# Kernel optimization log

Hardware: AMD Instinct MI355X
Metric: run time of the kernel (lower is better)

Reference implementation:

```python
import jax, jax.numpy as jnp
import numpy as np

N = 50000
E = 500000
IN_DIM = 384
HID = 128
HEADS = 4
OUT_DIM = 384
NEG_SLOPE = 0.2


def gat_conv(x, edge_index, W, att_src, att_dst, bias):
    """PyG GATConv (concat=True, add_self_loops=True, eval mode).
    x: [N, F_in]; edge_index: [2, E] (row 0 = source j, row 1 = target i);
    W: [F_in, H*C]; att_src/att_dst: [H, C]; bias: [H*C].
    """
    n = x.shape[0]
    # add self loops
    loops = jnp.arange(n, dtype=edge_index.dtype)
    src = jnp.concatenate([edge_index[0], loops])
    dst = jnp.concatenate([edge_index[1], loops])

    h = (x @ W).reshape(n, HEADS, -1)              # [N, H, C]
    a_src = jnp.einsum('nhc,hc->nh', h, att_src)   # [N, H]
    a_dst = jnp.einsum('nhc,hc->nh', h, att_dst)   # [N, H]

    e = a_src[src] + a_dst[dst]                    # [E', H]
    e = jax.nn.leaky_relu(e, NEG_SLOPE)
    # segment softmax over incoming edges of each target node
    e_max = jax.ops.segment_max(e, dst, num_segments=n)
    e_exp = jnp.exp(e - e_max[dst])
    denom = jax.ops.segment_sum(e_exp, dst, num_segments=n)
    alpha = e_exp / denom[dst]                     # [E', H]

    msg = h[src] * alpha[:, :, None]               # [E', H, C]
    out = jax.ops.segment_sum(msg, dst, num_segments=n)  # [N, H, C]
    return out.reshape(n, -1) + bias


def setup_inputs() -> dict:
    key = jax.random.key(0)
    ks = jax.random.split(key, 12)
    s_in = 1.0 / np.sqrt(IN_DIM)
    s_h = 1.0 / np.sqrt(HEADS * HID)
    return {
        'x': jax.random.normal(ks[0], (N, IN_DIM), dtype=jnp.float32),
        'edge_index': jax.random.randint(ks[1], (2, E), 0, N, dtype=jnp.int32),
        'W1': jax.random.normal(ks[2], (IN_DIM, HEADS * HID), dtype=jnp.float32) * s_in,
        'a1_src': jax.random.normal(ks[3], (HEADS, HID), dtype=jnp.float32) * s_in,
        'a1_dst': jax.random.normal(ks[4], (HEADS, HID), dtype=jnp.float32) * s_in,
        'b1': jnp.zeros((HEADS * HID,), dtype=jnp.float32),
        'W2': jax.random.normal(ks[5], (HEADS * HID, HEADS * HID), dtype=jnp.float32) * s_h,
        'a2_src': jax.random.normal(ks[6], (HEADS, HID), dtype=jnp.float32) * s_h,
        'a2_dst': jax.random.normal(ks[7], (HEADS, HID), dtype=jnp.float32) * s_h,
        'b2': jnp.zeros((HEADS * HID,), dtype=jnp.float32),
        'Wfc': jax.random.normal(ks[8], (HEADS * HID, OUT_DIM), dtype=jnp.float32) * s_h,
        'bfc': jnp.zeros((OUT_DIM,), dtype=jnp.float32),
    }


def reference(x, edge_index, W1, a1_src, a1_dst, b1, W2, a2_src, a2_dst, b2, Wfc, bfc):
    h = jax.nn.relu(gat_conv(x, edge_index, W1, a1_src, a1_dst, b1))
    h = jax.nn.relu(gat_conv(h, edge_index, W2, a2_src, a2_dst, b2))
    return h @ Wfc + bfc  # [N, OUT_DIM]
```

## Files before the change

### kernel.cpp

```cpp
#include <hip/hip_runtime.h>
#include <cfloat>
#include <cstdint>

#define HEADS 4
#define HIDC 128
#define HC 512
#define NEG 0.2f

typedef _Float16 half8 __attribute__((ext_vector_type(8)));
typedef float floatx4 __attribute__((ext_vector_type(4)));

__global__ __launch_bounds__(256) void mfma_gemm(
    const _Float16* __restrict__ A,
    const _Float16* __restrict__ Bt,
    _Float16* __restrict__ Ch,
    float* __restrict__ Cf,
    const float* __restrict__ bias,
    const float* __restrict__ atts,
    const float* __restrict__ attd,
    float* __restrict__ a_src,
    float* __restrict__ a_dst,
    int M, int N, int K, int Acb)
{
    __shared__ __align__(16) _Float16 As[128 * 64];
    __shared__ __align__(16) _Float16 Bs[128 * 64];

    const int nwg = gridDim.x * gridDim.y;
    int lin = blockIdx.y * gridDim.x + blockIdx.x;
    {
        const int q = nwg >> 3, r = nwg & 7;
        const int xcd = lin & 7, pos = lin >> 3;
        lin = (xcd < r ? xcd * (q + 1) : r * (q + 1) + (xcd - r) * q) + pos;
    }
    const int bx = lin % gridDim.x;
    const int by = lin / gridDim.x;

    const int tid = threadIdx.x;
    const int w = tid >> 6;
    const int lane = tid & 63;
    const int wr = (w >> 1) * 64;
    const int wc = (w & 1) * 64;

    const int rowBase = by * 128;
    const int colBase = bx * 128;

    const size_t Mp32 = (size_t)gridDim.y * 128 * 32;

    const int strow = lane >> 3;
    const int sColSw = ((lane & 7) ^ strow) * 8;

    const _Float16* gaP[4];
    const _Float16* gbP[4];
    _Float16* lA[4];
    _Float16* lB[4];
#pragma unroll
    for (int c = 0; c < 4; c++) {
        const int rr = c * 32 + w * 8;
        const int rA = rowBase + rr + strow;
        const int rB = colBase + rr + strow;
        gaP[c] = Acb ? (A + (size_t)(sColSw >> 5) * Mp32 + (size_t)rA * 32 + (sColSw & 31))
                     : (A + (size_t)rA * K + sColSw);
        gbP[c] = Bt + (size_t)rB * K + sColSw;
        lA[c] = &As[rr * 64];
        lB[c] = &Bs[rr * 64];
    }
    const size_t kA = Acb ? (Mp32 * 2) : (size_t)64;

    floatx4 acc[4][4];
#pragma unroll
    for (int i = 0; i < 4; i++)
#pragma unroll
        for (int j = 0; j < 4; j++) acc[i][j] = {0.f, 0.f, 0.f, 0.f};

    const int q16 = lane >> 4;
    const int l16 = lane & 15;

    for (int k0 = 0; k0 < K; k0 += 64) {
#pragma unroll
        for (int c = 0; c < 4; c++) {
            __builtin_amdgcn_global_load_lds(
                (const __attribute__((address_space(1))) unsigned int*)gaP[c],
                (__attribute__((address_space(3))) unsigned int*)lA[c], 16, 0, 0);
            __builtin_amdgcn_global_load_lds(
                (const __attribute__((address_space(1))) unsigned int*)gbP[c],
                (__attribute__((address_space(3))) unsigned int*)lB[c], 16, 0, 0);
            gaP[c] += kA;
            gbP[c] += 64;
        }
        __syncthreads();

#pragma unroll
        for (int s = 0; s < 2; s++) {
            half8 af[4], bf[4];
#pragma unroll
            for (int i = 0; i < 4; i++) {
                const int r = wr + i * 16 + l16;
                af[i] = *(const half8*)&As[r * 64 + (((s * 4 + q16) ^ (r & 7)) * 8)];
            }
#pragma unroll
            for (int j = 0; j < 4; j++) {
                const int r = wc + j * 16 + l16;
                bf[j] = *(const half8*)&Bs[r * 64 + (((s * 4 + q16) ^ (r & 7)) * 8)];
            }
#pragma unroll
            for (int i = 0; i < 4; i++)
#pragma unroll
                for (int j = 0; j < 4; j++)
                    acc[i][j] = __builtin_amdgcn_mfma_f32_16x16x32_f16(af[i], bf[j], acc[i][j], 0, 0, 0);
        }
        __syncthreads();
    }

    if (Ch) {
#pragma unroll
        for (int i = 0; i < 4; i++)
#pragma unroll
            for (int j = 0; j < 4; j++) {
                const int col = colBase + wc + j * 16 + l16;
                const size_t cbase = (size_t)(col >> 5) * Mp32 + (col & 31);
#pragma unroll
                for (int r = 0; r < 4; r++) {
                    const int row = rowBase + wr + i * 16 + q16 * 4 + r;
                    if (row < M) Ch[cbase + (size_t)row * 32] = (_Float16)acc[i][j][r];
                }
            }
    }
    if (Cf) {
#pragma unroll
        for (int i = 0; i < 4; i++)
#pragma unroll
            for (int j = 0; j < 4; j++) {
                const int col = colBase + wc + j * 16 + l16;
                const float bb = bias ? bias[col] : 0.f;
#pragma unroll
                for (int r = 0; r < 4; r++) {
                    const int row = rowBase + wr + i * 16 + q16 * 4 + r;
                    if (row < M) Cf[(size_t)row * N + col] = acc[i][j][r] + bb;
                }
            }
    }

    if (atts) {
        float* ps = (float*)As;
        float* pd = ps + 256;
        const int head = bx;
        float as[4], ad[4];
#pragma unroll
        for (int j = 0; j < 4; j++) {
            const int cl = wc + j * 16 + l16;
            as[j] = atts[head * HIDC + cl];
            ad[j] = attd[head * HIDC + cl];
        }
#pragma unroll
        for (int i = 0; i < 4; i++) {
#pragma unroll
            for (int r = 0; r < 4; r++) {
                float s_ = acc[i][0][r] * as[0] + acc[i][1][r] * as[1]
                         + acc[i][2][r] * as[2] + acc[i][3][r] * as[3];
                float d_ = acc[i][0][r] * ad[0] + acc[i][1][r] * ad[1]
                         + acc[i][2][r] * ad[2] + acc[i][3][r] * ad[3];
#pragma unroll
                for (int mk = 1; mk <= 8; mk <<= 1) {
                    s_ += __shfl_xor(s_, mk);
                    d_ += __shfl_xor(d_, mk);
                }
                if (l16 == 0) {
                    const int rloc = wr + i * 16 + q16 * 4 + r;
                    ps[(wc >> 6) * 128 + rloc] = s_;
                    pd[(wc >> 6) * 128 + rloc] = d_;
                }
            }
        }
        __syncthreads();
        if (tid < 128) {
            const int row = rowBase + tid;
            if (row < M) {
                a_src[(size_t)row * 4 + head] = ps[tid] + ps[128 + tid];
                a_dst[(size_t)row * 4 + head] = pd[tid] + pd[128 + tid];
            }
        }
    }
}

__global__ void convert_x_kernel(const float* __restrict__ x, _Float16* __restrict__ o, size_t nquads)
{
    size_t i = (size_t)blockIdx.x * blockDim.x + threadIdx.x;
    if (i < nquads) {
        float4 v = *(const float4*)(x + i * 4);
        _Float16* p = o + i * 4;
        p[0] = (_Float16)v.x; p[1] = (_Float16)v.y;
        p[2] = (_Float16)v.z; p[3] = (_Float16)v.w;
    }
}

__global__ void convert_wT3_kernel(
    const float* __restrict__ W1, const float* __restrict__ W2, const float* __restrict__ W3,
    _Float16* __restrict__ T1, _Float16* __restrict__ T2, _Float16* __restrict__ T3)
{
    const int z = blockIdx.z;
    const float* W = (z == 0) ? W1 : (z == 1) ? W2 : W3;
    _Float16* T = (z == 0) ? T1 : (z == 1) ? T2 : T3;
    const int K = (z == 0) ? 384 : 512;
    const int N = (z == 2) ? 384 : 512;
    int k = blockIdx.x * 64 + (threadIdx.x & 63);
    int n = blockIdx.y * 4 + (threadIdx.x >> 6);
    if (k < K && n < N) T[(size_t)n * K + k] = (_Float16)W[(size_t)k * N + n];
}

__global__ void count_kernel(const int* __restrict__ dst, int* __restrict__ deg, int E)
{
    int e = blockIdx.x * blockDim.x + threadIdx.x;
    if (e < E) atomicAdd(&deg[dst[e]], 1);
}

__global__ __launch_bounds__(256) void block_sum_kernel(
    const int* __restrict__ deg, int* __restrict__ bsum, int Nn)
{
    int gid = blockIdx.x * 256 + threadIdx.x;
    int v = (gid < Nn) ? deg[gid] : 0;
#pragma unroll
    for (int o = 32; o >= 1; o >>= 1) v += __shfl_xor(v, o);
    __shared__ int ws[4];
    if ((threadIdx.x & 63) == 0) ws[threadIdx.x >> 6] = v;
    __syncthreads();
    if (threadIdx.x == 0) bsum[blockIdx.x] = ws[0] + ws[1] + ws[2] + ws[3];
}

__global__ __launch_bounds__(256) void scan_bsum_kernel(
    const int* __restrict__ bsum, int* __restrict__ bbase, int nb)
{
    __shared__ int s[256];
    const int tid = threadIdx.x;
    int v = (tid < nb) ? bsum[tid] : 0;
    s[tid] = v;
    __syncthreads();
    for (int off = 1; off < 256; off <<= 1) {
        int t = (tid >= off) ? s[tid - off] : 0;
        __syncthreads();
        s[tid] += t;
        __syncthreads();
    }
    if (tid < nb) bbase[tid] = s[tid] - v;
}

__global__ __launch_bounds__(256) void fill_rowptr_kernel(
    const int* __restrict__ deg, const int* __restrict__ bbase,
    int* __restrict__ rowptr, int* __restrict__ cursor, int Nn, int E)
{
    __shared__ int s[256];
    const int tid = threadIdx.x;
    const int gid = blockIdx.x * 256 + tid;
    int v = (gid < Nn) ? deg[gid] : 0;
    s[tid] = v;
    __syncthreads();
    for (int off = 1; off < 256; off <<= 1) {
        int t = (tid >= off) ? s[tid - off] : 0;
        __syncthreads();
        s[tid] += t;
        __syncthreads();
    }
    if (gid < Nn) {
        int r = bbase[blockIdx.x] + s[tid] - v;
        rowptr[gid] = r;
        cursor[gid] = r;
    }
    if (gid == 0) rowptr[Nn] = E;
}

__global__ void fill_kernel(const int* __restrict__ src, const int* __restrict__ dst,
                            int* __restrict__ cursor, int* __restrict__ eidx,
                            int* __restrict__ edst, int E)
{
    int e = blockIdx.x * blockDim.x + threadIdx.x;
    if (e < E) {
        int d = dst[e];
        int pos = atomicAdd(&cursor[d], 1);
        eidx[pos] = src[e];
        edst[pos] = d;
    }
}

__global__ __launch_bounds__(256) void edge_weight_kernel(
    const int* __restrict__ eidx, const int* __restrict__ edst,
    const float* __restrict__ a_src, const float* __restrict__ a_dst,
    float* __restrict__ wH, float* __restrict__ wS, int E, int Ep, int Nn)
{
    int p = blockIdx.x * 256 + threadIdx.x;
    if (p < E) {
        int s = eidx[p];
        int d = edst[p];
        float4 as4 = *(const float4*)(a_src + (size_t)s * 4);
        float4 ad4 = *(const float4*)(a_dst + (size_t)d * 4);
        float l0 = as4.x + ad4.x; l0 = l0 > 0.f ? l0 : NEG * l0;
        float l1 = as4.y + ad4.y; l1 = l1 > 0.f ? l1 : NEG * l1;
        float l2 = as4.z + ad4.z; l2 = l2 > 0.f ? l2 : NEG * l2;
        float l3 = as4.w + ad4.w; l3 = l3 > 0.f ? l3 : NEG * l3;
        wH[0 * Ep + p] = __expf(l0);
        wH[1 * Ep + p] = __expf(l1);
        wH[2 * Ep + p] = __expf(l2);
        wH[3 * Ep + p] = __expf(l3);
    } else if (p < E + Nn) {
        int n = p - E;
        float4 as4 = *(const float4*)(a_src + (size_t)n * 4);
        float4 ad4 = *(const float4*)(a_dst + (size_t)n * 4);
        float l0 = as4.x + ad4.x; l0 = l0 > 0.f ? l0 : NEG * l0;
        float l1 = as4.y + ad4.y; l1 = l1 > 0.f ? l1 : NEG * l1;
        float l2 = as4.z + ad4.z; l2 = l2 > 0.f ? l2 : NEG * l2;
        float l3 = as4.w + ad4.w; l3 = l3 > 0.f ? l3 : NEG * l3;
        wS[0 * Nn + n] = __expf(l0);
        wS[1 * Nn + n] = __expf(l1);
        wS[2 * Nn + n] = __expf(l2);
        wS[3 * Nn + n] = __expf(l3);
    }
}

__global__ __launch_bounds__(256) void gather_kernel(
    const _Float16* __restrict__ h,
    const float* __restrict__ wH,
    const float* __restrict__ wS,
    const int* __restrict__ rowptr, const int* __restrict__ eidx,
    const float* __restrict__ bias, _Float16* __restrict__ out,
    int Nn, int Mp, int Ep, int nchunks)
{
    const int half = nchunks << 3;
    int lin = blockIdx.x;
    int cb;
    if (lin < half) { cb = lin & 7; }
    else { lin -= half; cb = 8 + (lin & 7); }
    const int chunk = lin >> 3;

    const int tid = threadIdx.x;
    const int wv = tid >> 6;
    const int lane = tid & 63;
    const int g = lane >> 2;
    const int l4 = lane & 3;
    const int node = chunk * 64 + wv * 16 + g;
    const bool valid = node < Nn;

    const int hd = cb >> 2;
    const size_t Mp32 = (size_t)Mp * 32;
    const _Float16* hs = h + (size_t)cb * Mp32 + l4 * 8;
    const float* wHp = wH + (size_t)hd * Ep;

    int beg = 0, deg = 0;
    float wSv = 0.f;
    if (valid) {
        beg = rowptr[node];
        deg = rowptr[node + 1] - beg;
        wSv = wS[(size_t)hd * Nn + node];
    }

    int mx = valid ? deg + 1 : 0;
#pragma unroll
    for (int m = 4; m <= 32; m <<= 1) {
        int o = __shfl_xor(mx, m);
        mx = o > mx ? o : mx;
    }

    float acc[8];
#pragma unroll
    for (int i = 0; i < 8; i++) acc[i] = 0.f;
    float dsum = 0.f;

    int sC = node;
    float wC = 0.f;
    if (0 < deg)      { sC = eidx[beg]; wC = wHp[beg]; }
    else if (0 == deg && valid) wC = wSv;

    for (int e = 0; e < mx; e++) {
        half8 hv = *(const half8*)(hs + (size_t)sC * 32);
        const float wf = wC;
        int sN = node;
        float wN = 0.f;
        const int en = e + 1;
        if (en < deg)       { sN = eidx[beg + en]; wN = wHp[beg + en]; }
        else if (en == deg && valid) wN = wSv;
        sC = sN; wC = wN;

        dsum += wf;
#pragma unroll
        for (int i = 0; i < 8; i++) acc[i] += wf * (float)hv[i];
    }

    if (valid) {
        const float is = 1.f / dsum;
        const float* bp = bias + cb * 32 + l4 * 8;
        half8 ov;
#pragma unroll
        for (int i = 0; i < 8; i++) {
            float o = acc[i] * is + bp[i];
            o = o > 0.f ? o : 0.f;
            ov[i] = (_Float16)o;
        }
        *(half8*)(out + (size_t)cb * Mp32 + (size_t)node * 32 + l4 * 8) = ov;
    }
}

extern "C" void kernel_launch(void* const* d_in, const int* in_sizes, int n_in,
                              void* d_out, int out_size, void* d_ws, size_t ws_size,
                              hipStream_t stream)
{
    const float* x   = (const float*)d_in[0];
    const int*   ei  = (const int*)d_in[1];
    const float* W1  = (const float*)d_in[2];
    const float* a1s = (const float*)d_in[3];
    const float* a1d = (const float*)d_in[4];
    const float* b1  = (const float*)d_in[5];
    const float* W2  = (const float*)d_in[6];
    const float* a2s = (const float*)d_in[7];
    const float* a2d = (const float*)d_in[8];
    const float* b2  = (const float*)d_in[9];
    const float* Wfc = (const float*)d_in[10];
    const float* bfc = (const float*)d_in[11];
    float* out = (float*)d_out;

    const int Nn  = in_sizes[0] / 384;
    const int E   = in_sizes[1] / 2;
    const int IN  = 384;
    const int OUT = in_sizes[11];
    const int Mp  = ((Nn + 127) / 128) * 128;
    const int nb  = (Nn + 255) / 256;
    const int Ep  = E + 16;

    uint8_t* p = (uint8_t*)d_ws;
    auto alloc = [&](size_t bytes) {
        uint8_t* r = p;
        p += (bytes + 255) & ~(size_t)255;
        return r;
    };
    _Float16* Ah_x = (_Float16*)alloc((size_t)Mp * IN * 2);
    _Float16* Ah_g = (_Float16*)alloc((size_t)Mp * HC * 2);
    _Float16* Hh   = (_Float16*)alloc((size_t)Mp * HC * 2);
    _Float16* Wt1  = (_Float16*)alloc((size_t)HC * IN * 2);
    _Float16* Wt2  = (_Float16*)alloc((size_t)HC * HC * 2);
    _Float16* Wt3  = (_Float16*)alloc((size_t)OUT * HC * 2);
    float* a_src   = (float*)alloc((size_t)Nn * 4 * 4);
    float* a_dst   = (float*)alloc((size_t)Nn * 4 * 4);
    int* deg       = (int*)alloc((size_t)Nn * 4);
    int* rowptr    = (int*)alloc((size_t)(Nn + 1) * 4);
    int* cursor    = (int*)alloc((size_t)Nn * 4);
    int* eidx      = (int*)alloc((size_t)Ep * 4);
    int* edst      = (int*)alloc((size_t)E * 4);
    float* wH      = (float*)alloc((size_t)4 * Ep * 4);
    float* wS      = (float*)alloc((size_t)4 * Nn * 4);
    int* bsum      = (int*)alloc((size_t)nb * 4);
    int* bbase     = (int*)alloc((size_t)nb * 4);

    const int* e_src = ei;
    const int* e_dst = ei + E;

    {
        size_t nq = (size_t)Nn * IN / 4;
        convert_x_kernel<<<(nq + 255) / 256, 256, 0, stream>>>(x, Ah_x, nq);
        dim3 gw(8, 128, 3);
        convert_wT3_kernel<<<gw, 256, 0, stream>>>(W1, W2, Wfc, Wt1, Wt2, Wt3);
    }

    hipMemsetAsync(deg, 0, Nn * sizeof(int), stream);
    const int eb = (E + 255) / 256;
    count_kernel<<<eb, 256, 0, stream>>>(e_dst, deg, E);
    block_sum_kernel<<<nb, 256, 0, stream>>>(deg, bsum, Nn);
    scan_bsum_kernel<<<1, 256, 0, stream>>>(bsum, bbase, nb);
    fill_rowptr_kernel<<<nb, 256, 0, stream>>>(deg, bbase, rowptr, cursor, Nn, E);
    fill_kernel<<<eb, 256, 0, stream>>>(e_src, e_dst, cursor, eidx, edst, E);

    const dim3 gg1(HC / 128, Mp / 128);
    const int nchunks = (Nn + 63) / 64;
    const int gwb = 16 * nchunks;
    const int ewb = (E + Nn + 255) / 256;

    mfma_gemm<<<gg1, 256, 0, stream>>>(Ah_x, Wt1, Hh, nullptr, nullptr,
                                       a1s, a1d, a_src, a_dst, Nn, HC, IN, 0);
    edge_weight_kernel<<<ewb, 256, 0, stream>>>(eidx, edst, a_src, a_dst, wH, wS, E, Ep, Nn);
    gather_kernel<<<gwb, 256, 0, stream>>>(Hh, wH, wS, rowptr, eidx, b1, Ah_g,
                                           Nn, Mp, Ep, nchunks);

    mfma_gemm<<<gg1, 256, 0, stream>>>(Ah_g, Wt2, Hh, nullptr, nullptr,
                                       a2s, a2d, a_src, a_dst, Nn, HC, HC, 1);
    edge_weight_kernel<<<ewb, 256, 0, stream>>>(eidx, edst, a_src, a_dst, wH, wS, E, Ep, Nn);
    gather_kernel<<<gwb, 256, 0, stream>>>(Hh, wH, wS, rowptr, eidx, b2, Ah_g,
                                           Nn, Mp, Ep, nchunks);

    const dim3 gg3(OUT / 128, Mp / 128);
    mfma_gemm<<<gg3, 256, 0, stream>>>(Ah_g, Wt3, nullptr, out, bfc,
                                       nullptr, nullptr, nullptr, nullptr, Nn, OUT, HC, 1);
}
```

Measured before the change: 559.5 us.

## Fold self-loops into CSR and unroll gather loop by four

Result: slower. 588.4 us (+5.2%).

```diff
diff --git a/kernel.cpp b/kernel.cpp
--- a/kernel.cpp
+++ b/kernel.cpp
@@ -217,7 +217,7 @@
     const int* __restrict__ deg, int* __restrict__ bsum, int Nn)
 {
     int gid = blockIdx.x * 256 + threadIdx.x;
-    int v = (gid < Nn) ? deg[gid] : 0;
+    int v = (gid < Nn) ? deg[gid] + 1 : 0;
 #pragma unroll
     for (int o = 32; o >= 1; o >>= 1) v += __shfl_xor(v, o);
     __shared__ int ws[4];
@@ -245,12 +245,13 @@
 
 __global__ __launch_bounds__(256) void fill_rowptr_kernel(
     const int* __restrict__ deg, const int* __restrict__ bbase,
-    int* __restrict__ rowptr, int* __restrict__ cursor, int Nn, int E)
+    int* __restrict__ rowptr, int* __restrict__ cursor,
+    int* __restrict__ eidx, int* __restrict__ edst, int Nn, int Et)
 {
     __shared__ int s[256];
     const int tid = threadIdx.x;
     const int gid = blockIdx.x * 256 + tid;
-    int v = (gid < Nn) ? deg[gid] : 0;
+    int v = (gid < Nn) ? deg[gid] + 1 : 0;
     s[tid] = v;
     __syncthreads();
     for (int off = 1; off < 256; off <<= 1) {
@@ -262,9 +263,11 @@
     if (gid < Nn) {
         int r = bbase[blockIdx.x] + s[tid] - v;
         rowptr[gid] = r;
-        cursor[gid] = r;
-    }
-    if (gid == 0) rowptr[Nn] = E;
+        cursor[gid] = r + 1;
+        eidx[r] = gid;
+        edst[r] = gid;
+    }
+    if (gid == 0) rowptr[Nn] = Et;
 }
 
 __global__ void fill_kernel(const int* __restrict__ src, const int* __restrict__ dst,
@@ -283,10 +286,10 @@
 __global__ __launch_bounds__(256) void edge_weight_kernel(
     const int* __restrict__ eidx, const int* __restrict__ edst,
     const float* __restrict__ a_src, const float* __restrict__ a_dst,
-    float* __restrict__ wH, float* __restrict__ wS, int E, int Ep, int Nn)
+    float* __restrict__ wH, int Et, int Ep)
 {
     int p = blockIdx.x * 256 + threadIdx.x;
-    if (p < E) {
+    if (p < Et) {
         int s = eidx[p];
         int d = edst[p];
         float4 as4 = *(const float4*)(a_src + (size_t)s * 4);
@@ -299,28 +302,15 @@
         wH[1 * Ep + p] = __expf(l1);
         wH[2 * Ep + p] = __expf(l2);
         wH[3 * Ep + p] = __expf(l3);
-    } else if (p < E + Nn) {
-        int n = p - E;
-        float4 as4 = *(const float4*)(a_src + (size_t)n * 4);
-        float4 ad4 = *(const float4*)(a_dst + (size_t)n * 4);
-        float l0 = as4.x + ad4.x; l0 = l0 > 0.f ? l0 : NEG * l0;
-        float l1 = as4.y + ad4.y; l1 = l1 > 0.f ? l1 : NEG * l1;
-        float l2 = as4.z + ad4.z; l2 = l2 > 0.f ? l2 : NEG * l2;
-        float l3 = as4.w + ad4.w; l3 = l3 > 0.f ? l3 : NEG * l3;
-        wS[0 * Nn + n] = __expf(l0);
-        wS[1 * Nn + n] = __expf(l1);
-        wS[2 * Nn + n] = __expf(l2);
-        wS[3 * Nn + n] = __expf(l3);
     }
 }
 
 __global__ __launch_bounds__(256) void gather_kernel(
     const _Float16* __restrict__ h,
     const float* __restrict__ wH,
-    const float* __restrict__ wS,
     const int* __restrict__ rowptr, const int* __restrict__ eidx,
     const float* __restrict__ bias, _Float16* __restrict__ out,
-    int Nn, int Mp, int Ep, int nchunks)
+    int Nn, int Mp, int Ep, int Et, int nchunks)
 {
     const int half = nchunks << 3;
     int lin = blockIdx.x;
@@ -337,49 +327,65 @@
     const int node = chunk * 64 + wv * 16 + g;
     const bool valid = node < Nn;
 
-    const int hd = cb >> 2;
     const size_t Mp32 = (size_t)Mp * 32;
     const _Float16* hs = h + (size_t)cb * Mp32 + l4 * 8;
-    const float* wHp = wH + (size_t)hd * Ep;
-
-    int beg = 0, deg = 0;
-    float wSv = 0.f;
+    const float* wHp = wH + (size_t)(cb >> 2) * Ep;
+    const int totM1 = Et - 1;
+
+    int beg = 0, cnt = 0;
     if (valid) {
         beg = rowptr[node];
-        deg = rowptr[node + 1] - beg;
-        wSv = wS[(size_t)hd * Nn + node];
-    }
-
-    int mx = valid ? deg + 1 : 0;
+        cnt = rowptr[node + 1] - beg;
+    }
+
+    int mx = cnt;
 #pragma unroll
     for (int m = 4; m <= 32; m <<= 1) {
         int o = __shfl_xor(mx, m);
         mx = o > mx ? o : mx;
     }
+    mx = (mx + 3) & ~3;
 
     float acc[8];
 #pragma unroll
     for (int i = 0; i < 8; i++) acc[i] = 0.f;
     float dsum = 0.f;
 
-    int sC = node;
-    float wC = 0.f;
-    if (0 < deg)      { sC = eidx[beg]; wC = wHp[beg]; }
-    else if (0 == deg && valid) wC = wSv;
-
-    for (int e = 0; e < mx; e++) {
-        half8 hv = *(const half8*)(hs + (size_t)sC * 32);
-        const float wf = wC;
-        int sN = node;
-        float wN = 0.f;
-        const int en = e + 1;
-        if (en < deg)       { sN = eidx[beg + en]; wN = wHp[beg + en]; }
-        else if (en == deg && valid) wN = wSv;
-        sC = sN; wC = wN;
-
-        dsum += wf;
-#pragma unroll
-        for (int i = 0; i < 8; i++) acc[i] += wf * (float)hv[i];
+    int s0, s1, s2, s3;
+    float w0, w1, w2, w3;
+    {
+        int p0 = min(beg + 0, totM1), p1 = min(beg + 1, totM1);
+        int p2 = min(beg + 2, totM1), p3 = min(beg + 3, totM1);
+        s0 = eidx[p0]; s1 = eidx[p1]; s2 = eidx[p2]; s3 = eidx[p3];
+        float a0 = wHp[p0], a1 = wHp[p1], a2 = wHp[p2], a3 = wHp[p3];
+        w0 = 0 < cnt ? a0 : 0.f;
+        w1 = 1 < cnt ? a1 : 0.f;
+        w2 = 2 < cnt ? a2 : 0.f;
+        w3 = 3 < cnt ? a3 : 0.f;
+    }
+
+    for (int e = 0; e < mx; e += 4) {
+        half8 hv0 = *(const half8*)(hs + (size_t)(s0 * 32));
+        half8 hv1 = *(const half8*)(hs + (size_t)(s1 * 32));
+        half8 hv2 = *(const half8*)(hs + (size_t)(s2 * 32));
+        half8 hv3 = *(const half8*)(hs + (size_t)(s3 * 32));
+        const int en = e + 4;
+        int p0 = min(beg + en + 0, totM1), p1 = min(beg + en + 1, totM1);
+        int p2 = min(beg + en + 2, totM1), p3 = min(beg + en + 3, totM1);
+        int n0 = eidx[p0], n1 = eidx[p1], n2 = eidx[p2], n3 = eidx[p3];
+        float a0 = wHp[p0], a1 = wHp[p1], a2 = wHp[p2], a3 = wHp[p3];
+        float x0 = en + 0 < cnt ? a0 : 0.f;
+        float x1 = en + 1 < cnt ? a1 : 0.f;
+        float x2 = en + 2 < cnt ? a2 : 0.f;
+        float x3 = en + 3 < cnt ? a3 : 0.f;
+
+        dsum += (w0 + w1) + (w2 + w3);
+#pragma unroll
+        for (int i = 0; i < 8; i++)
+            acc[i] += (w0 * (float)hv0[i] + w1 * (float)hv1[i])
+                    + (w2 * (float)hv2[i] + w3 * (float)hv3[i]);
+        s0 = n0; s1 = n1; s2 = n2; s3 = n3;
+        w0 = x0; w1 = x1; w2 = x2; w3 = x3;
     }
 
     if (valid) {
@@ -420,7 +426,8 @@
     const int OUT = in_sizes[11];
     const int Mp  = ((Nn + 127) / 128) * 128;
     const int nb  = (Nn + 255) / 256;
-    const int Ep  = E + 16;
+    const int Et  = E + Nn;
+    const int Ep  = (Et + 255) & ~255;
 
     uint8_t* p = (uint8_t*)d_ws;
     auto alloc = [&](size_t bytes) {
@@ -439,10 +446,9 @@
     int* deg       = (int*)alloc((size_t)Nn * 4);
     int* rowptr    = (int*)alloc((size_t)(Nn + 1) * 4);
     int* cursor    = (int*)alloc((size_t)Nn * 4);
-    int* eidx      = (int*)alloc((size_t)Ep * 4);
-    int* edst      = (int*)alloc((size_t)E * 4);
+    int* eidx      = (int*)alloc((size_t)Et * 4);
+    int* edst      = (int*)alloc((size_t)Et * 4);
     float* wH      = (float*)alloc((size_t)4 * Ep * 4);
-    float* wS      = (float*)alloc((size_t)4 * Nn * 4);
     int* bsum      = (int*)alloc((size_t)nb * 4);
     int* bbase     = (int*)alloc((size_t)nb * 4);
 
@@ -461,25 +467,25 @@
     count_kernel<<<eb, 256, 0, stream>>>(e_dst, deg, E);
     block_sum_kernel<<<nb, 256, 0, stream>>>(deg, bsum, Nn);
     scan_bsum_kernel<<<1, 256, 0, stream>>>(bsum, bbase, nb);
-    fill_rowptr_kernel<<<nb, 256, 0, stream>>>(deg, bbase, rowptr, cursor, Nn, E);
+    fill_rowptr_kernel<<<nb, 256, 0, stream>>>(deg, bbase, rowptr, cursor, eidx, edst, Nn, Et);
     fill_kernel<<<eb, 256, 0, stream>>>(e_src, e_dst, cursor, eidx, edst, E);
 
     const dim3 gg1(HC / 128, Mp / 128);
     const int nchunks = (Nn + 63) / 64;
     const int gwb = 16 * nchunks;
-    const int ewb = (E + Nn + 255) / 256;
+    const int ewb = (Et + 255) / 256;
 
     mfma_gemm<<<gg1, 256, 0, stream>>>(Ah_x, Wt1, Hh, nullptr, nullptr,
                                        a1s, a1d, a_src, a_dst, Nn, HC, IN, 0);
-    edge_weight_kernel<<<ewb, 256, 0, stream>>>(eidx, edst, a_src, a_dst, wH, wS, E, Ep, Nn);
-    gather_kernel<<<gwb, 256, 0, stream>>>(Hh, wH, wS, rowptr, eidx, b1, Ah_g,
-                                           Nn, Mp, Ep, nchunks);
+    edge_weight_kernel<<<ewb, 256, 0, stream>>>(eidx, edst, a_src, a_dst, wH, Et, Ep);
+    gather_kernel<<<gwb, 256, 0, stream>>>(Hh, wH, rowptr, eidx, b1, Ah_g,
+                                           Nn, Mp, Ep, Et, nchunks);
 
     mfma_gemm<<<gg1, 256, 0, stream>>>(Ah_g, Wt2, Hh, nullptr, nullptr,
                                        a2s, a2d, a_src, a_dst, Nn, HC, HC, 1);
-    edge_weight_kernel<<<ewb, 256, 0, stream>>>(eidx, edst, a_src, a_dst, wH, wS, E, Ep, Nn);
-    gather_kernel<<<gwb, 256, 0, stream>>>(Hh, wH, wS, rowptr, eidx, b2, Ah_g,
-                                           Nn, Mp, Ep, nchunks);
+    edge_weight_kernel<<<ewb, 256, 0, stream>>>(eidx, edst, a_src, a_dst, wH, Et, Ep);
+    gather_kernel<<<gwb, 256, 0, stream>>>(Hh, wH, rowptr, eidx, b2, Ah_g,
+                                           Nn, Mp, Ep, Et, nchunks);
 
     const dim3 gg3(OUT / 128, Mp / 128);
     mfma_gemm<<<gg3, 256, 0, stream>>>(Ah_g, Wt3, nullptr, out, bfc,
```
